# Kernel tuning notes

Measured on AMD Instinct MI355X. Metric: run time of the kernel, lower is better.

The kernel has to match this reference:

```python
import jax, jax.numpy as jnp
import numpy as np

N = 8192      # nodes
D_IN = 128    # input features
D_H = 48      # GAT hidden (hardcoded in module)
D_OUT = 32    # control output dim
NEG_INF = -9e15  # matches torch code's -9000000000000000.0


def setup_inputs() -> dict:
    key = jax.random.key(0)
    ks = jax.random.split(key, 12)
    s = 0.05
    return {
        "x": jax.random.normal(ks[0], (N, D_IN), jnp.float32),
        "adj": jax.random.randint(ks[1], (N, N), 0, 2, jnp.int32),
        "W_gat": jax.random.normal(ks[2], (D_H, D_IN), jnp.float32) * s,
        "a": jax.random.normal(ks[3], (1, D_H), jnp.float32) * s,
        "gamma": jnp.ones((D_H,), jnp.float32),
        "beta": jnp.zeros((D_H,), jnp.float32),
        "W1": jax.random.normal(ks[4], (256, D_H), jnp.float32) * s,
        "b1": jnp.zeros((256,), jnp.float32),
        "W2": jax.random.normal(ks[5], (128, 256), jnp.float32) * s,
        "b2": jnp.zeros((128,), jnp.float32),
        "W3": jax.random.normal(ks[6], (D_OUT, 128), jnp.float32) * s,
        "b3": jnp.zeros((D_OUT,), jnp.float32),
    }


def reference(x, adj, W_gat, a, gamma, beta, W1, b1, W2, b2, W3, b3):
    # --- LightweightGATLayer ---
    Wh = x @ W_gat.T                      # [N, D_H]
    s = Wh @ a.T                          # [N, 1] additive attention scores
    e = s + s.T                           # [N, N]
    e = jnp.where(e > 0, e, 0.2 * e)      # LeakyReLU(0.2)
    e = jnp.where(adj > 0, e, NEG_INF)    # mask non-edges
    attn = jax.nn.softmax(e, axis=1)      # row softmax; dropout is identity in eval
    h_prime = attn @ Wh                   # [N, D_H]
    # LayerNorm over last dim, eps=1e-5
    mu = jnp.mean(h_prime, axis=-1, keepdims=True)
    var = jnp.var(h_prime, axis=-1, keepdims=True)
    h = (h_prime - mu) * jax.lax.rsqrt(var + 1e-5) * gamma + beta
    # --- BiACT MLP head: 48 -> 256 -> 128 -> D_OUT ---
    h = jax.nn.relu(h @ W1.T + b1)
    h = jax.nn.relu(h @ W2.T + b2)
    return h @ W3.T + b3                  # [N, D_OUT]
```

## Files before the change

kernel.cpp:

```cpp
#include <hip/hip_runtime.h>

#define N 8192
#define DIN 128
#define DH 48
#define MT 128
#define KC 64
#define NSPLIT 8
#define JSPAN (N / NSPLIT)
#define NCHUNK (JSPAN / KC)
#define NW64 (N / 64)
#define ACC_STRIDE 64
#define HSTR 49
#define RB 32

typedef _Float16 half8 __attribute__((ext_vector_type(8)));
typedef float f32x4 __attribute__((ext_vector_type(4)));

__global__ __launch_bounds__(256) void k_pack(const int* __restrict__ adj,
                                              unsigned long long* __restrict__ mask) {
    int t = threadIdx.x;
    int lane = t & 63, w = t >> 6;
    size_t wid = (size_t)blockIdx.x * 4 + w;
    size_t base = wid * 64;
    const int* src = adj + base * 64 + lane;
    #pragma unroll 4
    for (int k = 0; k < 64; ++k) {
        int v = src[(size_t)k * 64];
        unsigned long long b = __ballot(v != 0);
        if (lane == 0) mask[base + k] = b;
    }
}

__global__ __launch_bounds__(256) void k_wh(const float* __restrict__ x,
                                            const float* __restrict__ Wg,
                                            float* __restrict__ Wh) {
    __shared__ float wT[DIN * DH];
    int t = threadIdx.x;
    for (int e = t; e < DIN * DH; e += 256) {
        int c = e / DIN, k = e % DIN;
        wT[k * DH + c] = Wg[e];
    }
    __syncthreads();
    int o = blockIdx.x * 256 + t;
    int r = o / DH, c = o % DH;
    const float4* xr = (const float4*)(x + (size_t)r * DIN);
    float acc = 0.f;
    #pragma unroll 8
    for (int k4 = 0; k4 < DIN / 4; ++k4) {
        float4 xv = xr[k4];
        int kb = k4 * 4;
        acc += xv.x * wT[(kb + 0) * DH + c];
        acc += xv.y * wT[(kb + 1) * DH + c];
        acc += xv.z * wT[(kb + 2) * DH + c];
        acc += xv.w * wT[(kb + 3) * DH + c];
    }
    Wh[o] = acc;
}

__global__ __launch_bounds__(256) void k_s(const float* __restrict__ Wh,
                                           const float* __restrict__ a,
                                           float* __restrict__ s) {
    int r = blockIdx.x * 256 + threadIdx.x;
    const float4* wr = (const float4*)(Wh + (size_t)r * DH);
    const float4* av = (const float4*)a;
    float acc = 0.f;
    #pragma unroll
    for (int k4 = 0; k4 < DH / 4; ++k4) {
        float4 w = wr[k4]; float4 aa = av[k4];
        acc += w.x * aa.x + w.y * aa.y + w.z * aa.z + w.w * aa.w;
    }
    s[r] = acc;
}

__global__ __launch_bounds__(256) void k_tr(const float* __restrict__ Wh,
                                            _Float16* __restrict__ WhT) {
    __shared__ _Float16 tile[DH][72];
    int t = threadIdx.x;
    int r0 = blockIdx.x * 64;
    for (int e = t; e < 64 * DH; e += 256) {
        int r = e / DH, c = e % DH;
        tile[c][r] = (_Float16)Wh[(size_t)(r0 + r) * DH + c];
    }
    __syncthreads();
    for (int u = t; u < DH * 8; u += 256) {
        int c = u >> 3, g = u & 7;
        *(half8*)&WhT[(size_t)c * N + r0 + g * 8] = *(const half8*)&tile[c][g * 8];
    }
}

__device__ inline half8 mk_p(float si, float4 sa, float4 sb, unsigned mb) {
    float e0 = si + sa.x, e1 = si + sa.y, e2 = si + sa.z, e3 = si + sa.w;
    float e4 = si + sb.x, e5 = si + sb.y, e6 = si + sb.z, e7 = si + sb.w;
    e0 = fmaxf(e0, 0.2f * e0); e1 = fmaxf(e1, 0.2f * e1);
    e2 = fmaxf(e2, 0.2f * e2); e3 = fmaxf(e3, 0.2f * e3);
    e4 = fmaxf(e4, 0.2f * e4); e5 = fmaxf(e5, 0.2f * e5);
    e6 = fmaxf(e6, 0.2f * e6); e7 = fmaxf(e7, 0.2f * e7);
    half8 r;
    r[0] = (_Float16)((mb & 1u)   ? __expf(e0) : 0.f);
    r[1] = (_Float16)((mb & 2u)   ? __expf(e1) : 0.f);
    r[2] = (_Float16)((mb & 4u)   ? __expf(e2) : 0.f);
    r[3] = (_Float16)((mb & 8u)   ? __expf(e3) : 0.f);
    r[4] = (_Float16)((mb & 16u)  ? __expf(e4) : 0.f);
    r[5] = (_Float16)((mb & 32u)  ? __expf(e5) : 0.f);
    r[6] = (_Float16)((mb & 64u)  ? __expf(e6) : 0.f);
    r[7] = (_Float16)((mb & 128u) ? __expf(e7) : 0.f);
    return r;
}

__global__ __launch_bounds__(256, 4) void k_gat(const unsigned long long* __restrict__ mask,
                                                const _Float16* __restrict__ WhT,
                                                const float* __restrict__ s,
                                                float* __restrict__ accWs) {
    int t = threadIdx.x;
    int tile = blockIdx.x & 63;
    int split = blockIdx.x >> 6;
    int i0 = tile * MT;
    int jbase = split * JSPAN;

    int lane = t & 63, w = t >> 6;
    int ln16 = lane & 15, kq = lane >> 4;

    half8 bc;
    {
        _Float16 v = (ln16 == 0) ? (_Float16)1.0f : (_Float16)0.0f;
        #pragma unroll
        for (int i = 0; i < 8; ++i) bc[i] = v;
    }

    f32x4 acc[2][4];
    #pragma unroll
    for (int m = 0; m < 2; ++m)
        #pragma unroll
        for (int n = 0; n < 4; ++n) acc[m][n] = (f32x4){0.f, 0.f, 0.f, 0.f};

    const int row0 = i0 + w * 32 + ln16;
    const int row1 = row0 + 16;
    const float si0 = s[row0];
    const float si1 = s[row1];
    const unsigned long long* mr0 = mask + (size_t)row0 * NW64 + (jbase >> 6);
    const unsigned long long* mr1 = mask + (size_t)row1 * NW64 + (jbase >> 6);

    for (int chunk = 0; chunk < NCHUNK; ++chunk) {
        const int j0 = jbase + chunk * KC;
        const int jk0 = j0 + kq * 8;
        const int jk1 = jk0 + 32;

        unsigned long long mw0 = mr0[chunk];
        unsigned long long mw1 = mr1[chunk];
        float4 s0a = *(const float4*)(s + jk0);
        float4 s0b = *(const float4*)(s + jk0 + 4);
        float4 s1a = *(const float4*)(s + jk1);
        float4 s1b = *(const float4*)(s + jk1 + 4);
        half8 bf00 = *(const half8*)&WhT[(size_t)(0  + ln16) * N + jk0];
        half8 bf01 = *(const half8*)&WhT[(size_t)(16 + ln16) * N + jk0];
        half8 bf02 = *(const half8*)&WhT[(size_t)(32 + ln16) * N + jk0];
        half8 bf10 = *(const half8*)&WhT[(size_t)(0  + ln16) * N + jk1];
        half8 bf11 = *(const half8*)&WhT[(size_t)(16 + ln16) * N + jk1];
        half8 bf12 = *(const half8*)&WhT[(size_t)(32 + ln16) * N + jk1];

        unsigned b00 = (unsigned)(mw0 >> (kq * 8)) & 0xffu;
        unsigned b01 = (unsigned)(mw0 >> (kq * 8 + 32)) & 0xffu;
        unsigned b10 = (unsigned)(mw1 >> (kq * 8)) & 0xffu;
        unsigned b11 = (unsigned)(mw1 >> (kq * 8 + 32)) & 0xffu;

        half8 a00 = mk_p(si0, s0a, s0b, b00);
        half8 a01 = mk_p(si0, s1a, s1b, b01);
        half8 a10 = mk_p(si1, s0a, s0b, b10);
        half8 a11 = mk_p(si1, s1a, s1b, b11);

        acc[0][0] = __builtin_amdgcn_mfma_f32_16x16x32_f16(a00, bf00, acc[0][0], 0, 0, 0);
        acc[0][1] = __builtin_amdgcn_mfma_f32_16x16x32_f16(a00, bf01, acc[0][1], 0, 0, 0);
        acc[0][2] = __builtin_amdgcn_mfma_f32_16x16x32_f16(a00, bf02, acc[0][2], 0, 0, 0);
        acc[0][3] = __builtin_amdgcn_mfma_f32_16x16x32_f16(a00, bc,   acc[0][3], 0, 0, 0);
        acc[1][0] = __builtin_amdgcn_mfma_f32_16x16x32_f16(a10, bf00, acc[1][0], 0, 0, 0);
        acc[1][1] = __builtin_amdgcn_mfma_f32_16x16x32_f16(a10, bf01, acc[1][1], 0, 0, 0);
        acc[1][2] = __builtin_amdgcn_mfma_f32_16x16x32_f16(a10, bf02, acc[1][2], 0, 0, 0);
        acc[1][3] = __builtin_amdgcn_mfma_f32_16x16x32_f16(a10, bc,   acc[1][3], 0, 0, 0);
        acc[0][0] = __builtin_amdgcn_mfma_f32_16x16x32_f16(a01, bf10, acc[0][0], 0, 0, 0);
        acc[0][1] = __builtin_amdgcn_mfma_f32_16x16x32_f16(a01, bf11, acc[0][1], 0, 0, 0);
        acc[0][2] = __builtin_amdgcn_mfma_f32_16x16x32_f16(a01, bf12, acc[0][2], 0, 0, 0);
        acc[0][3] = __builtin_amdgcn_mfma_f32_16x16x32_f16(a01, bc,   acc[0][3], 0, 0, 0);
        acc[1][0] = __builtin_amdgcn_mfma_f32_16x16x32_f16(a11, bf10, acc[1][0], 0, 0, 0);
        acc[1][1] = __builtin_amdgcn_mfma_f32_16x16x32_f16(a11, bf11, acc[1][1], 0, 0, 0);
        acc[1][2] = __builtin_amdgcn_mfma_f32_16x16x32_f16(a11, bf12, acc[1][2], 0, 0, 0);
        acc[1][3] = __builtin_amdgcn_mfma_f32_16x16x32_f16(a11, bc,   acc[1][3], 0, 0, 0);
    }

    #pragma unroll
    for (int mtl = 0; mtl < 2; ++mtl) {
        size_t rbase = (size_t)split * N + i0 + w * 32 + mtl * 16 + kq * 4;
        #pragma unroll
        for (int nt = 0; nt < 4; ++nt) {
            int col = nt * 16 + ln16;
            if (nt == 3 && ln16 != 0) continue;
            #pragma unroll
            for (int reg = 0; reg < 4; ++reg)
                accWs[(rbase + reg) * ACC_STRIDE + col] = acc[mtl][nt][reg];
        }
    }
}

__global__ __launch_bounds__(256) void k_mlp(const float* __restrict__ accWs,
                                             const float* __restrict__ gamma,
                                             const float* __restrict__ beta,
                                             const float* __restrict__ W1, const float* __restrict__ b1,
                                             const float* __restrict__ W2, const float* __restrict__ b2,
                                             const float* __restrict__ W3, const float* __restrict__ b3,
                                             float* __restrict__ out) {
    __shared__ float hs[RB * HSTR];
    __shared__ float hN[RB * DH];
    __shared__ float h1[RB * 256];
    __shared__ float h2[RB * 128];
    int t = threadIdx.x;
    int r0 = blockIdx.x * RB;

    for (int e = t; e < RB * HSTR; e += 256) {
        int r = e / HSTR, d = e % HSTR;
        size_t base = (size_t)(r0 + r) * ACC_STRIDE + d;
        float v = 0.f;
        #pragma unroll
        for (int sp = 0; sp < NSPLIT; ++sp)
            v += accWs[(size_t)sp * N * ACC_STRIDE + base];
        hs[e] = v;
    }
    __syncthreads();

    if (t < RB) {
        float invl = 1.f / hs[t * HSTR + 48];
        float sum = 0.f;
        for (int d = 0; d < DH; ++d) sum += hs[t * HSTR + d];
        float mean = sum * invl * (1.f / DH);
        float var = 0.f;
        for (int d = 0; d < DH; ++d) {
            float dv = hs[t * HSTR + d] * invl - mean;
            var += dv * dv;
        }
        var *= (1.f / DH);
        float rs = rsqrtf(var + 1e-5f);
        for (int d = 0; d < DH; ++d) {
            float hv = (hs[t * HSTR + d] * invl - mean) * rs;
            hN[t * DH + d] = hv * gamma[d] + beta[d];
        }
    }
    __syncthreads();

    {
        int c0 = (t & 127) * 2, c1 = c0 + 1;
        int rbeg = (t >> 7) * 16;
        float4 wa[12], wb[12];
        const float4* wr0 = (const float4*)(W1 + c0 * DH);
        const float4* wr1 = (const float4*)(W1 + c1 * DH);
        #pragma unroll
        for (int k4 = 0; k4 < 12; ++k4) { wa[k4] = wr0[k4]; wb[k4] = wr1[k4]; }
        float ba = b1[c0], bb = b1[c1];
        for (int r = rbeg; r < rbeg + 16; ++r) {
            const float4* hv4 = (const float4*)&hN[r * DH];
            float a0 = ba, a1 = bb;
            #pragma unroll
            for (int k4 = 0; k4 < 12; ++k4) {
                float4 hv = hv4[k4];
                a0 += hv.x * wa[k4].x + hv.y * wa[k4].y + hv.z * wa[k4].z + hv.w * wa[k4].w;
                a1 += hv.x * wb[k4].x + hv.y * wb[k4].y + hv.z * wb[k4].z + hv.w * wb[k4].w;
            }
            h1[r * 256 + c0] = fmaxf(a0, 0.f);
            h1[r * 256 + c1] = fmaxf(a1, 0.f);
        }
    }
    __syncthreads();

    {
        int c4 = (t & 31) * 4;
        int rr0 = (t >> 5) * 4;
        float a[4][4];
        #pragma unroll
        for (int rr = 0; rr < 4; ++rr)
            #pragma unroll
            for (int cc = 0; cc < 4; ++cc) a[rr][cc] = 0.f;
        for (int k4 = 0; k4 < 64; ++k4) {
            float4 h[4], wv[4];
            #pragma unroll
            for (int rr = 0; rr < 4; ++rr)
                h[rr] = *(const float4*)&h1[(rr0 + rr) * 256 + 4 * k4];
            #pragma unroll
            for (int cc = 0; cc < 4; ++cc)
                wv[cc] = *(const float4*)&W2[(size_t)(c4 + cc) * 256 + 4 * k4];
            #pragma unroll
            for (int rr = 0; rr < 4; ++rr)
                #pragma unroll
                for (int cc = 0; cc < 4; ++cc)
                    a[rr][cc] += h[rr].x * wv[cc].x + h[rr].y * wv[cc].y
                               + h[rr].z * wv[cc].z + h[rr].w * wv[cc].w;
        }
        #pragma unroll
        for (int rr = 0; rr < 4; ++rr)
            #pragma unroll
            for (int cc = 0; cc < 4; ++cc)
                h2[(rr0 + rr) * 128 + c4 + cc] = fmaxf(a[rr][cc] + b2[c4 + cc], 0.f);
    }
    __syncthreads();

    {
        int c = t & 31;
        int rr0 = (t >> 5) * 4;
        float a[4];
        float bias = b3[c];
        #pragma unroll
        for (int rr = 0; rr < 4; ++rr) a[rr] = bias;
        const float4* wrow = (const float4*)(W3 + c * 128);
        for (int k4 = 0; k4 < 32; ++k4) {
            float4 wv = wrow[k4];
            #pragma unroll
            for (int rr = 0; rr < 4; ++rr) {
                float4 hv = *(const float4*)&h2[(rr0 + rr) * 128 + 4 * k4];
                a[rr] += wv.x * hv.x + wv.y * hv.y + wv.z * hv.z + wv.w * hv.w;
            }
        }
        #pragma unroll
        for (int rr = 0; rr < 4; ++rr)
            out[(size_t)(r0 + rr0 + rr) * 32 + c] = a[rr];
    }
}

extern "C" void kernel_launch(void* const* d_in, const int* in_sizes, int n_in,
                              void* d_out, int out_size, void* d_ws, size_t ws_size,
                              hipStream_t stream) {
    const float* x     = (const float*)d_in[0];
    const int*   adj   = (const int*)d_in[1];
    const float* Wg    = (const float*)d_in[2];
    const float* a     = (const float*)d_in[3];
    const float* gamma = (const float*)d_in[4];
    const float* beta  = (const float*)d_in[5];
    const float* W1    = (const float*)d_in[6];
    const float* b1    = (const float*)d_in[7];
    const float* W2    = (const float*)d_in[8];
    const float* b2    = (const float*)d_in[9];
    const float* W3    = (const float*)d_in[10];
    const float* b3    = (const float*)d_in[11];
    float* out = (float*)d_out;

    float* ws = (float*)d_ws;
    float*              Wh    = ws;
    float*              s     = Wh + (size_t)N * DH;
    _Float16*           WhT   = (_Float16*)(s + N);
    unsigned long long* mask  = (unsigned long long*)(WhT + (size_t)N * DH);
    float*              accWs = (float*)(mask + (size_t)N * NW64);

    k_pack<<<N * N / 64 / 256, 256, 0, stream>>>(adj, mask);
    k_wh<<<N * DH / 256, 256, 0, stream>>>(x, Wg, Wh);
    k_s<<<N / 256, 256, 0, stream>>>(Wh, a, s);
    k_tr<<<N / 64, 256, 0, stream>>>(Wh, WhT);
    k_gat<<<64 * NSPLIT, 256, 0, stream>>>(mask, WhT, s, accWs);
    k_mlp<<<N / RB, 256, 0, stream>>>(accWs, gamma, beta, W1, b1, W2, b2, W3, b3, out);
}
```

Baseline: 518.1 us.

## Stage attention tiles and Wh chunks in LDS, drop transpose kernel, double splits

The GAT kernel now builds each 128x64 tile of exp-scores once into shared memory, with two threads per row, and converts and transposes each Wh chunk into shared memory inside the loop. This replaces the separate transpose kernel and the per-lane global fragment loads. NSPLIT doubles to 16 to launch more blocks. The cost is two barriers per chunk, extra LDS traffic, and larger partial-accumulator output for k_mlp to reduce, which must also handle the new split count.

```diff
diff --git a/kernel.cpp b/kernel.cpp
--- a/kernel.cpp
+++ b/kernel.cpp
@@ -5,7 +5,8 @@
 #define DH 48
 #define MT 128
 #define KC 64
-#define NSPLIT 8
+#define PSTR 72
+#define NSPLIT 16
 #define JSPAN (N / NSPLIT)
 #define NCHUNK (JSPAN / KC)
 #define NW64 (N / 64)
@@ -70,22 +71,6 @@
         acc += w.x * aa.x + w.y * aa.y + w.z * aa.z + w.w * aa.w;
     }
     s[r] = acc;
-}
-
-__global__ __launch_bounds__(256) void k_tr(const float* __restrict__ Wh,
-                                            _Float16* __restrict__ WhT) {
-    __shared__ _Float16 tile[DH][72];
-    int t = threadIdx.x;
-    int r0 = blockIdx.x * 64;
-    for (int e = t; e < 64 * DH; e += 256) {
-        int r = e / DH, c = e % DH;
-        tile[c][r] = (_Float16)Wh[(size_t)(r0 + r) * DH + c];
-    }
-    __syncthreads();
-    for (int u = t; u < DH * 8; u += 256) {
-        int c = u >> 3, g = u & 7;
-        *(half8*)&WhT[(size_t)c * N + r0 + g * 8] = *(const half8*)&tile[c][g * 8];
-    }
 }
 
 __device__ inline half8 mk_p(float si, float4 sa, float4 sb, unsigned mb) {
@@ -108,17 +93,24 @@
 }
 
 __global__ __launch_bounds__(256, 4) void k_gat(const unsigned long long* __restrict__ mask,
-                                                const _Float16* __restrict__ WhT,
+                                                const float* __restrict__ Wh,
                                                 const float* __restrict__ s,
                                                 float* __restrict__ accWs) {
+    __shared__ _Float16 pS[MT][PSTR];
+    __shared__ _Float16 wS[64][PSTR];
     int t = threadIdx.x;
     int tile = blockIdx.x & 63;
     int split = blockIdx.x >> 6;
     int i0 = tile * MT;
     int jbase = split * JSPAN;
+    int jw0 = jbase >> 6;
 
     int lane = t & 63, w = t >> 6;
     int ln16 = lane & 15, kq = lane >> 4;
+    int prow = t >> 1, ph = t & 1;
+
+    for (int e = t; e < 16 * PSTR; e += 256)
+        wS[48 + e / PSTR][e % PSTR] = (_Float16)0.0f;
 
     half8 bc;
     {
@@ -133,57 +125,54 @@
         #pragma unroll
         for (int n = 0; n < 4; ++n) acc[m][n] = (f32x4){0.f, 0.f, 0.f, 0.f};
 
-    const int row0 = i0 + w * 32 + ln16;
-    const int row1 = row0 + 16;
-    const float si0 = s[row0];
-    const float si1 = s[row1];
-    const unsigned long long* mr0 = mask + (size_t)row0 * NW64 + (jbase >> 6);
-    const unsigned long long* mr1 = mask + (size_t)row1 * NW64 + (jbase >> 6);
+    const float si = s[i0 + prow];
+    const unsigned long long* mrow = mask + (size_t)(i0 + prow) * NW64 + jw0;
+
+    __syncthreads();
 
     for (int chunk = 0; chunk < NCHUNK; ++chunk) {
         const int j0 = jbase + chunk * KC;
-        const int jk0 = j0 + kq * 8;
-        const int jk1 = jk0 + 32;
-
-        unsigned long long mw0 = mr0[chunk];
-        unsigned long long mw1 = mr1[chunk];
-        float4 s0a = *(const float4*)(s + jk0);
-        float4 s0b = *(const float4*)(s + jk0 + 4);
-        float4 s1a = *(const float4*)(s + jk1);
-        float4 s1b = *(const float4*)(s + jk1 + 4);
-        half8 bf00 = *(const half8*)&WhT[(size_t)(0  + ln16) * N + jk0];
-        half8 bf01 = *(const half8*)&WhT[(size_t)(16 + ln16) * N + jk0];
-        half8 bf02 = *(const half8*)&WhT[(size_t)(32 + ln16) * N + jk0];
-        half8 bf10 = *(const half8*)&WhT[(size_t)(0  + ln16) * N + jk1];
-        half8 bf11 = *(const half8*)&WhT[(size_t)(16 + ln16) * N + jk1];
-        half8 bf12 = *(const half8*)&WhT[(size_t)(32 + ln16) * N + jk1];
-
-        unsigned b00 = (unsigned)(mw0 >> (kq * 8)) & 0xffu;
-        unsigned b01 = (unsigned)(mw0 >> (kq * 8 + 32)) & 0xffu;
-        unsigned b10 = (unsigned)(mw1 >> (kq * 8)) & 0xffu;
-        unsigned b11 = (unsigned)(mw1 >> (kq * 8 + 32)) & 0xffu;
-
-        half8 a00 = mk_p(si0, s0a, s0b, b00);
-        half8 a01 = mk_p(si0, s1a, s1b, b01);
-        half8 a10 = mk_p(si1, s0a, s0b, b10);
-        half8 a11 = mk_p(si1, s1a, s1b, b11);
-
-        acc[0][0] = __builtin_amdgcn_mfma_f32_16x16x32_f16(a00, bf00, acc[0][0], 0, 0, 0);
-        acc[0][1] = __builtin_amdgcn_mfma_f32_16x16x32_f16(a00, bf01, acc[0][1], 0, 0, 0);
-        acc[0][2] = __builtin_amdgcn_mfma_f32_16x16x32_f16(a00, bf02, acc[0][2], 0, 0, 0);
-        acc[0][3] = __builtin_amdgcn_mfma_f32_16x16x32_f16(a00, bc,   acc[0][3], 0, 0, 0);
-        acc[1][0] = __builtin_amdgcn_mfma_f32_16x16x32_f16(a10, bf00, acc[1][0], 0, 0, 0);
-        acc[1][1] = __builtin_amdgcn_mfma_f32_16x16x32_f16(a10, bf01, acc[1][1], 0, 0, 0);
-        acc[1][2] = __builtin_amdgcn_mfma_f32_16x16x32_f16(a10, bf02, acc[1][2], 0, 0, 0);
-        acc[1][3] = __builtin_amdgcn_mfma_f32_16x16x32_f16(a10, bc,   acc[1][3], 0, 0, 0);
-        acc[0][0] = __builtin_amdgcn_mfma_f32_16x16x32_f16(a01, bf10, acc[0][0], 0, 0, 0);
-        acc[0][1] = __builtin_amdgcn_mfma_f32_16x16x32_f16(a01, bf11, acc[0][1], 0, 0, 0);
-        acc[0][2] = __builtin_amdgcn_mfma_f32_16x16x32_f16(a01, bf12, acc[0][2], 0, 0, 0);
-        acc[0][3] = __builtin_amdgcn_mfma_f32_16x16x32_f16(a01, bc,   acc[0][3], 0, 0, 0);
-        acc[1][0] = __builtin_amdgcn_mfma_f32_16x16x32_f16(a11, bf10, acc[1][0], 0, 0, 0);
-        acc[1][1] = __builtin_amdgcn_mfma_f32_16x16x32_f16(a11, bf11, acc[1][1], 0, 0, 0);
-        acc[1][2] = __builtin_amdgcn_mfma_f32_16x16x32_f16(a11, bf12, acc[1][2], 0, 0, 0);
-        acc[1][3] = __builtin_amdgcn_mfma_f32_16x16x32_f16(a11, bc,   acc[1][3], 0, 0, 0);
+        {
+            const float* wsrc = Wh + (size_t)j0 * DH;
+            #pragma unroll
+            for (int k = 0; k < 12; ++k) {
+                int e = t + k * 256;
+                int jc = e / DH, d = e % DH;
+                wS[d][jc] = (_Float16)wsrc[e];
+            }
+        }
+        {
+            unsigned long long mw = mrow[chunk];
+            #pragma unroll
+            for (int g = 0; g < 4; ++g) {
+                int jo = ph * 32 + g * 8;
+                float4 sa = *(const float4*)(s + j0 + jo);
+                float4 sb = *(const float4*)(s + j0 + jo + 4);
+                unsigned mb = (unsigned)(mw >> jo) & 0xffu;
+                half8 pv = mk_p(si, sa, sb, mb);
+                *(half8*)&pS[prow][jo] = pv;
+            }
+        }
+        __syncthreads();
+        {
+            int m0 = w * 32;
+            #pragma unroll
+            for (int kt = 0; kt < 2; ++kt) {
+                int kk = kt * 32 + kq * 8;
+                half8 b0 = *(const half8*)&wS[0  + ln16][kk];
+                half8 b1 = *(const half8*)&wS[16 + ln16][kk];
+                half8 b2 = *(const half8*)&wS[32 + ln16][kk];
+                #pragma unroll
+                for (int mtl = 0; mtl < 2; ++mtl) {
+                    half8 a = *(const half8*)&pS[m0 + mtl * 16 + ln16][kk];
+                    acc[mtl][0] = __builtin_amdgcn_mfma_f32_16x16x32_f16(a, b0, acc[mtl][0], 0, 0, 0);
+                    acc[mtl][1] = __builtin_amdgcn_mfma_f32_16x16x32_f16(a, b1, acc[mtl][1], 0, 0, 0);
+                    acc[mtl][2] = __builtin_amdgcn_mfma_f32_16x16x32_f16(a, b2, acc[mtl][2], 0, 0, 0);
+                    acc[mtl][3] = __builtin_amdgcn_mfma_f32_16x16x32_f16(a, bc, acc[mtl][3], 0, 0, 0);
+                }
+            }
+        }
+        __syncthreads();
     }
 
     #pragma unroll
@@ -341,14 +330,12 @@
     float* ws = (float*)d_ws;
     float*              Wh    = ws;
     float*              s     = Wh + (size_t)N * DH;
-    _Float16*           WhT   = (_Float16*)(s + N);
-    unsigned long long* mask  = (unsigned long long*)(WhT + (size_t)N * DH);
+    unsigned long long* mask  = (unsigned long long*)(s + N);
     float*              accWs = (float*)(mask + (size_t)N * NW64);
 
     k_pack<<<N * N / 64 / 256, 256, 0, stream>>>(adj, mask);
     k_wh<<<N * DH / 256, 256, 0, stream>>>(x, Wg, Wh);
     k_s<<<N / 256, 256, 0, stream>>>(Wh, a, s);
-    k_tr<<<N / 64, 256, 0, stream>>>(Wh, WhT);
-    k_gat<<<64 * NSPLIT, 256, 0, stream>>>(mask, WhT, s, accWs);
+    k_gat<<<64 * NSPLIT, 256, 0, stream>>>(mask, Wh, s, accWs);
     k_mlp<<<N / RB, 256, 0, stream>>>(accWs, gamma, beta, W1, b1, W2, b2, W3, b3, out);
 }
```

Measured after the change: 509.6 us. Within noise of the previous version (-1.6%).
